# Kernel tuning notes

Measured on AMD Instinct MI355X. Metric: run time of the kernel, lower is better.

Reference implementation:

```python
import jax, jax.numpy as jnp
import numpy as np

EPS = 1e-12  # torch F.normalize default eps

def _l2norm(x):
    # torch.nn.functional.normalize(x, dim=-1): x / max(||x||_2, eps)
    n = jnp.linalg.norm(x, axis=-1, keepdims=True)
    return x / jnp.maximum(n, EPS)

def setup_inputs() -> dict:
    key = jax.random.key(0)
    ks = jax.random.split(key, 12)
    B, T, D, V, C = 16, 2048, 1024, 32000, 6
    s = 0.02
    text = jax.random.randint(ks[0], (B * T,), 0, V, dtype=jnp.int64)
    offsets = (jnp.arange(B, dtype=jnp.int64) * T)  # uniform-length sequences
    emb = jax.random.normal(ks[1], (V, D), dtype=jnp.float32) * s
    Wq = jax.random.normal(ks[2], (D, D), dtype=jnp.float32) * s
    bq = jnp.zeros((D,), jnp.float32)
    Wk = jax.random.normal(ks[3], (D, D), dtype=jnp.float32) * s
    bk = jnp.zeros((D,), jnp.float32)
    Wv = jax.random.normal(ks[4], (D, D), dtype=jnp.float32) * s
    bv = jnp.zeros((D,), jnp.float32)
    Wfc = jax.random.normal(ks[5], (D, D), dtype=jnp.float32) * s
    bfc = jnp.zeros((D,), jnp.float32)
    Wo = jax.random.normal(ks[6], (C, D), dtype=jnp.float32) * s
    bo = jnp.zeros((C,), jnp.float32)
    return {"text": text, "offsets": offsets, "emb": emb,
            "Wq": Wq, "bq": bq, "Wk": Wk, "bk": bk, "Wv": Wv, "bv": bv,
            "Wfc": Wfc, "bfc": bfc, "Wo": Wo, "bo": bo}

def reference(text, offsets, emb, Wq, bq, Wk, bk, Wv, bv, Wfc, bfc, Wo, bo):
    B = offsets.shape[0]
    T = text.shape[0] // B  # uniform lengths -> pad_sequence == reshape
    D = emb.shape[1]
    tok = text.reshape(B, T)
    x = emb[tok]                                   # [B,T,D]
    q = x @ Wq.T + bq
    k = x @ Wk.T + bk
    v = x @ Wv.T + bv
    scores = jnp.einsum('bqd,bkd->bqk', q, k) / jnp.sqrt(jnp.asarray(D, x.dtype))
    causal = jnp.tril(jnp.ones((T, T), dtype=bool))
    scores = jnp.where(causal[None, :, :], scores, -jnp.inf)
    attn = jax.nn.softmax(scores, axis=-1)
    out = jnp.einsum('bqk,bkd->bqd', attn, v) + x  # residual with embedding
    out = _l2norm(out)
    out = out + (out @ Wfc.T + bfc)                # residual FFN
    out = _l2norm(out)
    last = out[:, -1, :]                           # [B,D]
    return jax.nn.sigmoid(last @ Wo.T + bo)        # [B,num_class]
```

## Files before the change

kernel.cpp:

```cpp
#include <hip/hip_runtime.h>
#include <hip/hip_bf16.h>
#include <math.h>

typedef unsigned short ushort_t;

__device__ __forceinline__ float bf2f(ushort_t u) {
    union { unsigned int i; float f; } v;
    v.i = ((unsigned int)u) << 16;
    return v.f;
}

__device__ __forceinline__ ushort_t f2bf(float f) {
    union { float f; unsigned int i; } v; v.f = f;
    unsigned int lsb = (v.i >> 16) & 1;
    unsigned int r = v.i + 0x7FFF + lsb;
    return (ushort_t)(r >> 16);
}

__device__ __forceinline__ float wave_sum(float acc) {
    #pragma unroll
    for (int off = 32; off >= 1; off >>= 1) acc += __shfl_xor(acc, off, 64);
    return acc;
}
__device__ __forceinline__ float wave_max(float acc) {
    #pragma unroll
    for (int off = 32; off >= 1; off >>= 1) acc = fmaxf(acc, __shfl_xor(acc, off, 64));
    return acc;
}

__device__ __forceinline__ void ld8(const void* p, int isbf, size_t i, float* o) {
    if (isbf) {
        uint4 raw = *reinterpret_cast<const uint4*>((const ushort_t*)p + i);
        const ushort_t* pu = reinterpret_cast<const ushort_t*>(&raw);
        #pragma unroll
        for (int k = 0; k < 8; ++k) o[k] = bf2f(pu[k]);
    } else {
        const float4* f = reinterpret_cast<const float4*>((const float*)p + i);
        float4 a = f[0], b = f[1];
        o[0]=a.x; o[1]=a.y; o[2]=a.z; o[3]=a.w;
        o[4]=b.x; o[5]=b.y; o[6]=b.z; o[7]=b.w;
    }
}

__device__ __forceinline__ void ld4(const void* p, int isbf, size_t i, float* o) {
    if (isbf) {
        uint2 raw = *reinterpret_cast<const uint2*>((const ushort_t*)p + i);
        const ushort_t* pu = reinterpret_cast<const ushort_t*>(&raw);
        #pragma unroll
        for (int k = 0; k < 4; ++k) o[k] = bf2f(pu[k]);
    } else {
        float4 a = *reinterpret_cast<const float4*>((const float*)p + i);
        o[0]=a.x; o[1]=a.y; o[2]=a.z; o[3]=a.w;
    }
}

__device__ __forceinline__ float ldS(const void* p, int isbf, size_t i) {
    return isbf ? bf2f(((const ushort_t*)p)[i]) : ((const float*)p)[i];
}

__device__ __forceinline__ int tokAt(const void* text, int isi64, size_t i) {
    return isi64 ? ((const int*)text)[2 * i] : ((const int*)text)[i];
}

__device__ __forceinline__ void detect_flags(const void* emb, const void* text, int* sf) {
    if (threadIdx.x < 64) {
        const int lane = threadIdx.x;
        ushort_t u = ((const ushort_t*)emb)[2 * lane];
        int e = (u >> 7) & 0xFF;
        unsigned long long mb = __ballot(e >= 0x60 && e <= 0x7E);
        int odd = ((const int*)text)[2 * lane + 1];
        unsigned long long mi = __ballot(odd != 0);
        if (lane == 0) {
            sf[0] = (__popcll(mb) >= 32) ? 1 : 0;
            sf[1] = (__popcll(mi) == 0) ? 1 : 0;
        }
    }
    __syncthreads();
}

__device__ __forceinline__ void hoist16(const float* v, int lane, float* c16) {
    #pragma unroll
    for (int k = 0; k < 16; ++k) c16[k] = v[lane * 16 + k];
}

__global__ void kQC(const void* __restrict__ text, const void* __restrict__ emb,
                    const void* __restrict__ Wq, const void* __restrict__ bq,
                    const void* __restrict__ Wk, float* __restrict__ c_part,
                    int B, int T, int D) {
    const int ch = blockIdx.x / B;
    const int b  = blockIdx.x % B;
    const int i0 = ch << 6;
    const int tid = threadIdx.x;
    __shared__ int sf[2];
    __shared__ float xs[1024];
    __shared__ float qs[64];
    detect_flags(emb, text, sf);
    const int isbf = sf[0], isi64 = sf[1];
    const int tok = tokAt(text, isi64, (size_t)b * T + (T - 1));
    float w4[4];
    {
        const int dd = tid * 4;
        ld4(emb, isbf, (size_t)tok * D + dd, w4);
        xs[dd]=w4[0]; xs[dd+1]=w4[1]; xs[dd+2]=w4[2]; xs[dd+3]=w4[3];
    }
    __syncthreads();
    const int wave = tid >> 6, lane = tid & 63;
    float c16[16];
    hoist16(xs, lane, c16);
    float w[8];
    for (int r = 0; r < 16; ++r) {
        const int i = i0 + wave * 16 + r;
        float acc = 0.f;
        ld8(Wq, isbf, (size_t)i * D + lane * 16, w);
        #pragma unroll
        for (int k = 0; k < 8; ++k) acc += w[k] * c16[k];
        ld8(Wq, isbf, (size_t)i * D + lane * 16 + 8, w);
        #pragma unroll
        for (int k = 0; k < 8; ++k) acc += w[k] * c16[8 + k];
        acc = wave_sum(acc);
        if (lane == 0) qs[wave * 16 + r] = acc + ldS(bq, isbf, i);
    }
    __syncthreads();
    const int d = tid * 4;
    float a0=0.f, a1=0.f, a2=0.f, a3=0.f;
    #pragma unroll 8
    for (int i = 0; i < 64; ++i) {
        const float qv = qs[i];
        ld4(Wk, isbf, (size_t)(i0 + i) * D + d, w4);
        a0 += qv*w4[0]; a1 += qv*w4[1]; a2 += qv*w4[2]; a3 += qv*w4[3];
    }
    *reinterpret_cast<float4*>(c_part + ((size_t)ch * B + b) * D + d)
        = make_float4(a0, a1, a2, a3);
}

__global__ void kCC(const float* __restrict__ c_part, float* __restrict__ c,
                    int B, int D, int nch) {
    const int nb = D >> 8;
    const int b = blockIdx.x / nb;
    const int d = (blockIdx.x % nb) * 256 + threadIdx.x;
    float acc = 0.f;
    for (int cc = 0; cc < nch; ++cc)
        acc += c_part[((size_t)cc * B + b) * D + d];
    c[(size_t)b * D + d] = acc;
}

__global__ void k35(const void* __restrict__ text, const void* __restrict__ emb,
                    const float* __restrict__ c, float* __restrict__ xbar_part,
                    float* __restrict__ m_part, float* __restrict__ l_part,
                    int B, int T, int D, float scale) {
    const int nchT = T >> 5;
    const int b = blockIdx.x / nchT;
    const int ch = blockIdx.x % nchT;
    const int j0 = ch << 5;
    const int tid = threadIdx.x;
    __shared__ int sf[2];
    __shared__ ushort_t rows[32 * 1024];
    __shared__ float cs[1024];
    __shared__ float sjs[32];
    __shared__ float wls[32];
    __shared__ int tks[32];
    detect_flags(emb, text, sf);
    const int isbf = sf[0], isi64 = sf[1];
    {
        const int d = tid * 4;
        float4 v = *reinterpret_cast<const float4*>(c + (size_t)b * D + d);
        cs[d]=v.x; cs[d+1]=v.y; cs[d+2]=v.z; cs[d+3]=v.w;
    }
    if (tid < 32) tks[tid] = tokAt(text, isi64, (size_t)b * T + j0 + tid);
    __syncthreads();
    if (isbf) {
        const ushort_t* E = (const ushort_t*)emb;
        const int half = tid >> 7;
        const int off  = (tid & 127) * 8;
        #pragma unroll 4
        for (int sw = 0; sw < 16; ++sw) {
            const int r = sw * 2 + half;
            uint4 v = *reinterpret_cast<const uint4*>(E + (size_t)tks[r] * D + off);
            *reinterpret_cast<uint4*>(&rows[r * 1024 + off]) = v;
        }
    }
    __syncthreads();
    const int wave = tid >> 6, lane = tid & 63;
    {
        float c16[16];
        hoist16(cs, lane, c16);
        float w[8];
        for (int rr = 0; rr < 8; ++rr) {
            const int r = wave + rr * 4;
            float acc = 0.f;
            if (isbf) {
                uint4 raw = *reinterpret_cast<const uint4*>(&rows[r * 1024 + lane * 16]);
                const ushort_t* pu = reinterpret_cast<const ushort_t*>(&raw);
                #pragma unroll
                for (int k = 0; k < 8; ++k) acc += bf2f(pu[k]) * c16[k];
                raw = *reinterpret_cast<const uint4*>(&rows[r * 1024 + lane * 16 + 8]);
                #pragma unroll
                for (int k = 0; k < 8; ++k) acc += bf2f(pu[k]) * c16[8 + k];
            } else {
                ld8(emb, 0, (size_t)tks[r] * D + lane * 16, w);
                #pragma unroll
                for (int k = 0; k < 8; ++k) acc += w[k] * c16[k];
                ld8(emb, 0, (size_t)tks[r] * D + lane * 16 + 8, w);
                #pragma unroll
                for (int k = 0; k < 8; ++k) acc += w[k] * c16[8 + k];
            }
            acc = wave_sum(acc);
            if (lane == 0) sjs[r] = acc * scale;
        }
    }
    __syncthreads();
    float mx = -INFINITY;
    #pragma unroll
    for (int j = 0; j < 32; ++j) mx = fmaxf(mx, sjs[j]);
    if (tid < 32) wls[tid] = expf(sjs[tid] - mx);
    __syncthreads();
    if (tid < 64) {
        float v = (tid < 32) ? wls[tid] : 0.f;
        v = wave_sum(v);
        if (tid == 0) { m_part[(size_t)b * nchT + ch] = mx;
                        l_part[(size_t)b * nchT + ch] = v; }
    }
    const int d = tid * 4;
    float a0=0.f, a1=0.f, a2=0.f, a3=0.f;
    if (isbf) {
        #pragma unroll 8
        for (int j = 0; j < 32; ++j) {
            const float wj = wls[j];
            uint2 raw = *reinterpret_cast<const uint2*>(&rows[j * 1024 + d]);
            const ushort_t* pu = reinterpret_cast<const ushort_t*>(&raw);
            a0 += wj*bf2f(pu[0]); a1 += wj*bf2f(pu[1]);
            a2 += wj*bf2f(pu[2]); a3 += wj*bf2f(pu[3]);
        }
    } else {
        float w4[4];
        #pragma unroll 8
        for (int j = 0; j < 32; ++j) {
            const float wj = wls[j];
            ld4(emb, 0, (size_t)tks[j] * D + d, w4);
            a0 += wj*w4[0]; a1 += wj*w4[1]; a2 += wj*w4[2]; a3 += wj*w4[3];
        }
    }
    *reinterpret_cast<float4*>(xbar_part + ((size_t)b * nchT + ch) * D + d)
        = make_float4(a0, a1, a2, a3);
}

__global__ void kC(const float* __restrict__ xbar_part, const float* __restrict__ m_part,
                   const float* __restrict__ l_part, float* __restrict__ xbar,
                   int B, int D, int nchT) {
    const int nb = D >> 8;
    const int b = blockIdx.x / nb;
    const int d = (blockIdx.x % nb) * 256 + threadIdx.x;
    __shared__ float sc[128];
    if (threadIdx.x < 64) {
        float mx = -INFINITY;
        for (int cc = (int)threadIdx.x; cc < nchT; cc += 64)
            mx = fmaxf(mx, m_part[(size_t)b * nchT + cc]);
        mx = wave_max(mx);
        float ls = 0.f;
        for (int cc = (int)threadIdx.x; cc < nchT; cc += 64)
            ls += l_part[(size_t)b * nchT + cc] * expf(m_part[(size_t)b * nchT + cc] - mx);
        ls = wave_sum(ls);
        for (int cc = (int)threadIdx.x; cc < nchT; cc += 64)
            sc[cc] = expf(m_part[(size_t)b * nchT + cc] - mx) / ls;
    }
    __syncthreads();
    float acc = 0.f;
    for (int cc = 0; cc < nchT; ++cc)
        acc += sc[cc] * xbar_part[((size_t)b * nchT + cc) * D + d];
    xbar[(size_t)b * D + d] = acc;
}

__global__ void kVA(const void* __restrict__ text, const void* __restrict__ emb,
                    const void* __restrict__ Wv, const void* __restrict__ bv,
                    const float* __restrict__ xbar, float* __restrict__ u,
                    int B, int T, int D) {
    const int ch = blockIdx.x / B;
    const int b  = blockIdx.x % B;
    const int r0 = ch << 5;
    const int tid = threadIdx.x;
    __shared__ int sf[2];
    __shared__ float xb[1024];
    __shared__ float xl[32];
    detect_flags(emb, text, sf);
    const int isbf = sf[0], isi64 = sf[1];
    const int tok = tokAt(text, isi64, (size_t)b * T + (T - 1));
    if (tid < 32) xl[tid] = ldS(emb, isbf, (size_t)tok * D + r0 + tid);
    {
        const int dd = tid * 4;
        float4 v = *reinterpret_cast<const float4*>(xbar + (size_t)b * D + dd);
        xb[dd]=v.x; xb[dd+1]=v.y; xb[dd+2]=v.z; xb[dd+3]=v.w;
    }
    __syncthreads();
    const int wave = tid >> 6, lane = tid & 63;
    float c16[16];
    hoist16(xb, lane, c16);
    float w[8];
    for (int rr = 0; rr < 8; ++rr) {
        const int i = r0 + wave + rr * 4;
        float acc = 0.f;
        ld8(Wv, isbf, (size_t)i * D + lane * 16, w);
        #pragma unroll
        for (int k = 0; k < 8; ++k) acc += w[k] * c16[k];
        ld8(Wv, isbf, (size_t)i * D + lane * 16 + 8, w);
        #pragma unroll
        for (int k = 0; k < 8; ++k) acc += w[k] * c16[8 + k];
        acc = wave_sum(acc);
        if (lane == 0) u[(size_t)b * D + i] = acc + ldS(bv, isbf, i) + xl[i - r0];
    }
}

__global__ void k6c_h2(const void* __restrict__ text, const void* __restrict__ emb,
                       const void* __restrict__ Wfc, const void* __restrict__ bfc,
                       const float* __restrict__ u, float* __restrict__ h2,
                       int B, int D) {
    const int ch = blockIdx.x / B;
    const int b  = blockIdx.x % B;
    const int r0 = ch << 5;
    const int tid = threadIdx.x;
    __shared__ int sf[2];
    __shared__ float hs[1024];
    __shared__ float red[256];
    __shared__ float s_rn;
    detect_flags(emb, text, sf);
    const int isbf = sf[0];
    float part;
    {
        const int dd = tid * 4;
        float4 v = *reinterpret_cast<const float4*>(u + (size_t)b * D + dd);
        hs[dd]=v.x; hs[dd+1]=v.y; hs[dd+2]=v.z; hs[dd+3]=v.w;
        part = v.x*v.x + v.y*v.y + v.z*v.z + v.w*v.w;
    }
    red[tid] = part;
    __syncthreads();
    for (int st = 128; st; st >>= 1) {
        if (tid < st) red[tid] += red[tid + st];
        __syncthreads();
    }
    if (tid == 0) s_rn = 1.f / fmaxf(sqrtf(red[0]), 1e-12f);
    __syncthreads();
    const float rn = s_rn;
    {
        const int dd = tid * 4;
        hs[dd] *= rn; hs[dd+1] *= rn; hs[dd+2] *= rn; hs[dd+3] *= rn;
    }
    __syncthreads();
    const int wave = tid >> 6, lane = tid & 63;
    float c16[16];
    hoist16(hs, lane, c16);
    float w[8];
    for (int rr = 0; rr < 8; ++rr) {
        const int i = r0 + wave + rr * 4;
        float acc = 0.f;
        ld8(Wfc, isbf, (size_t)i * D + lane * 16, w);
        #pragma unroll
        for (int k = 0; k < 8; ++k) acc += w[k] * c16[k];
        ld8(Wfc, isbf, (size_t)i * D + lane * 16 + 8, w);
        #pragma unroll
        for (int k = 0; k < 8; ++k) acc += w[k] * c16[8 + k];
        acc = wave_sum(acc);
        if (lane == 0) h2[(size_t)b * D + i] = hs[i] + acc + ldS(bfc, isbf, i);
    }
}

__global__ void k6d_out(const void* __restrict__ text, const void* __restrict__ emb,
                        const void* __restrict__ Wo, const void* __restrict__ bo,
                        const float* __restrict__ h2, void* __restrict__ out,
                        int D, int C, int total) {
    __shared__ int sf[2];
    detect_flags(emb, text, sf);
    const int isbf = sf[0];
    const int g = blockIdx.x * 4 + (threadIdx.x >> 6);
    if (g >= total) return;
    const int lane = threadIdx.x & 63;
    const int b = g / C, ci = g % C;
    float a1 = 0.f, a2 = 0.f, w[8], h[8];
    for (int d0 = lane * 8; d0 < D; d0 += 512) {
        ld8(Wo, isbf, (size_t)ci * D + d0, w);
        ld8(h2, 0, (size_t)b * D + d0, h);
        #pragma unroll
        for (int k = 0; k < 8; ++k) { a1 += w[k] * h[k]; a2 += h[k] * h[k]; }
    }
    a1 = wave_sum(a1);
    a2 = wave_sum(a2);
    if (lane == 0) {
        float rn = 1.f / fmaxf(sqrtf(a2), 1e-12f);
        float z = a1 * rn + ldS(bo, isbf, ci);
        float y = 1.f / (1.f + expf(-z));
        if (isbf) ((ushort_t*)out)[g] = f2bf(y);
        else      ((float*)out)[g] = y;
    }
}

extern "C" void kernel_launch(void* const* d_in, const int* in_sizes, int n_in,
                              void* d_out, int out_size, void* d_ws, size_t ws_size,
                              hipStream_t stream) {
    const void* text = d_in[0];
    const void* emb = d_in[2];
    const void* Wq  = d_in[3];
    const void* bq  = d_in[4];
    const void* Wk  = d_in[5];
    const void* Wv  = d_in[7];
    const void* bv  = d_in[8];
    const void* Wfc = d_in[9];
    const void* bfc = d_in[10];
    const void* Wo  = d_in[11];
    const void* bo  = d_in[12];

    const int B = in_sizes[1];
    const int T = in_sizes[0] / B;
    const int D = in_sizes[4];
    const int C = in_sizes[12];

    const int nch_c = D / 64;
    const int nchT  = T / 32;

    float* ws        = (float*)d_ws;
    float* c_part    = ws;
    float* c         = c_part + (size_t)nch_c * B * D;
    float* xbar_part = c + (size_t)B * D;
    float* m_part    = xbar_part + (size_t)B * nchT * D;
    float* l_part    = m_part + (size_t)B * nchT;
    float* xbar      = l_part + (size_t)B * nchT;
    float* u         = xbar + (size_t)B * D;
    float* h2        = u + (size_t)B * D;

    const float scale = 1.0f / sqrtf((float)D);

    kQC<<<(D / 64) * B, 256, 0, stream>>>(text, emb, Wq, bq, Wk, c_part, B, T, D);
    kCC<<<B * (D / 256), 256, 0, stream>>>(c_part, c, B, D, nch_c);
    k35<<<B * (T / 32), 256, 0, stream>>>(text, emb, c, xbar_part, m_part, l_part,
                                          B, T, D, scale);
    kC<<<B * (D / 256), 256, 0, stream>>>(xbar_part, m_part, l_part, xbar, B, D, nchT);
    kVA<<<(D / 32) * B, 256, 0, stream>>>(text, emb, Wv, bv, xbar, u, B, T, D);
    k6c_h2<<<(D / 32) * B, 256, 0, stream>>>(text, emb, Wfc, bfc, u, h2, B, D);
    k6d_out<<<(B * C + 3) / 4, 256, 0, stream>>>(text, emb, Wo, bo, h2, d_out, D, C, B * C);
}
```

Before: 300.7 us.

## Halve chunk sizes in QC and attention kernels, split combine reductions across waves

```diff
diff --git a/kernel.cpp b/kernel.cpp
--- a/kernel.cpp
+++ b/kernel.cpp
@@ -89,11 +89,11 @@
                     int B, int T, int D) {
     const int ch = blockIdx.x / B;
     const int b  = blockIdx.x % B;
-    const int i0 = ch << 6;
+    const int i0 = ch << 5;
     const int tid = threadIdx.x;
     __shared__ int sf[2];
     __shared__ float xs[1024];
-    __shared__ float qs[64];
+    __shared__ float qs[32];
     detect_flags(emb, text, sf);
     const int isbf = sf[0], isi64 = sf[1];
     const int tok = tokAt(text, isi64, (size_t)b * T + (T - 1));
@@ -108,8 +108,8 @@
     float c16[16];
     hoist16(xs, lane, c16);
     float w[8];
-    for (int r = 0; r < 16; ++r) {
-        const int i = i0 + wave * 16 + r;
+    for (int r = 0; r < 8; ++r) {
+        const int i = i0 + wave * 8 + r;
         float acc = 0.f;
         ld8(Wq, isbf, (size_t)i * D + lane * 16, w);
         #pragma unroll
@@ -118,13 +118,13 @@
         #pragma unroll
         for (int k = 0; k < 8; ++k) acc += w[k] * c16[8 + k];
         acc = wave_sum(acc);
-        if (lane == 0) qs[wave * 16 + r] = acc + ldS(bq, isbf, i);
+        if (lane == 0) qs[wave * 8 + r] = acc + ldS(bq, isbf, i);
     }
     __syncthreads();
     const int d = tid * 4;
     float a0=0.f, a1=0.f, a2=0.f, a3=0.f;
     #pragma unroll 8
-    for (int i = 0; i < 64; ++i) {
+    for (int i = 0; i < 32; ++i) {
         const float qv = qs[i];
         ld4(Wk, isbf, (size_t)(i0 + i) * D + d, w4);
         a0 += qv*w4[0]; a1 += qv*w4[1]; a2 += qv*w4[2]; a3 += qv*w4[3];
@@ -135,30 +135,38 @@
 
 __global__ void kCC(const float* __restrict__ c_part, float* __restrict__ c,
                     int B, int D, int nch) {
-    const int nb = D >> 8;
+    const int nb = D >> 6;
     const int b = blockIdx.x / nb;
-    const int d = (blockIdx.x % nb) * 256 + threadIdx.x;
+    const int dblk = blockIdx.x % nb;
+    const int q = threadIdx.x >> 6, dl = threadIdx.x & 63;
+    const int d = dblk * 64 + dl;
+    __shared__ float red[256];
+    const int per = nch >> 2;
     float acc = 0.f;
-    for (int cc = 0; cc < nch; ++cc)
+    for (int j = 0; j < per; ++j) {
+        const int cc = q * per + j;
         acc += c_part[((size_t)cc * B + b) * D + d];
-    c[(size_t)b * D + d] = acc;
+    }
+    red[threadIdx.x] = acc;
+    __syncthreads();
+    if (q == 0) c[(size_t)b * D + d] = red[dl] + red[64 + dl] + red[128 + dl] + red[192 + dl];
 }
 
 __global__ void k35(const void* __restrict__ text, const void* __restrict__ emb,
                     const float* __restrict__ c, float* __restrict__ xbar_part,
                     float* __restrict__ m_part, float* __restrict__ l_part,
                     int B, int T, int D, float scale) {
-    const int nchT = T >> 5;
+    const int nchT = T >> 4;
     const int b = blockIdx.x / nchT;
     const int ch = blockIdx.x % nchT;
-    const int j0 = ch << 5;
+    const int j0 = ch << 4;
     const int tid = threadIdx.x;
     __shared__ int sf[2];
-    __shared__ ushort_t rows[32 * 1024];
+    __shared__ ushort_t rows[16 * 1024];
     __shared__ float cs[1024];
-    __shared__ float sjs[32];
-    __shared__ float wls[32];
-    __shared__ int tks[32];
+    __shared__ float sjs[16];
+    __shared__ float wls[16];
+    __shared__ int tks[16];
     detect_flags(emb, text, sf);
     const int isbf = sf[0], isi64 = sf[1];
     {
@@ -166,14 +174,14 @@
         float4 v = *reinterpret_cast<const float4*>(c + (size_t)b * D + d);
         cs[d]=v.x; cs[d+1]=v.y; cs[d+2]=v.z; cs[d+3]=v.w;
     }
-    if (tid < 32) tks[tid] = tokAt(text, isi64, (size_t)b * T + j0 + tid);
+    if (tid < 16) tks[tid] = tokAt(text, isi64, (size_t)b * T + j0 + tid);
     __syncthreads();
     if (isbf) {
         const ushort_t* E = (const ushort_t*)emb;
         const int half = tid >> 7;
         const int off  = (tid & 127) * 8;
-        #pragma unroll 4
-        for (int sw = 0; sw < 16; ++sw) {
+        #pragma unroll
+        for (int sw = 0; sw < 8; ++sw) {
             const int r = sw * 2 + half;
             uint4 v = *reinterpret_cast<const uint4*>(E + (size_t)tks[r] * D + off);
             *reinterpret_cast<uint4*>(&rows[r * 1024 + off]) = v;
@@ -185,7 +193,7 @@
         float c16[16];
         hoist16(cs, lane, c16);
         float w[8];
-        for (int rr = 0; rr < 8; ++rr) {
+        for (int rr = 0; rr < 4; ++rr) {
             const int r = wave + rr * 4;
             float acc = 0.f;
             if (isbf) {
@@ -211,11 +219,11 @@
     __syncthreads();
     float mx = -INFINITY;
     #pragma unroll
-    for (int j = 0; j < 32; ++j) mx = fmaxf(mx, sjs[j]);
-    if (tid < 32) wls[tid] = expf(sjs[tid] - mx);
+    for (int j = 0; j < 16; ++j) mx = fmaxf(mx, sjs[j]);
+    if (tid < 16) wls[tid] = expf(sjs[tid] - mx);
     __syncthreads();
     if (tid < 64) {
-        float v = (tid < 32) ? wls[tid] : 0.f;
+        float v = (tid < 16) ? wls[tid] : 0.f;
         v = wave_sum(v);
         if (tid == 0) { m_part[(size_t)b * nchT + ch] = mx;
                         l_part[(size_t)b * nchT + ch] = v; }
@@ -223,8 +231,8 @@
     const int d = tid * 4;
     float a0=0.f, a1=0.f, a2=0.f, a3=0.f;
     if (isbf) {
-        #pragma unroll 8
-        for (int j = 0; j < 32; ++j) {
+        #pragma unroll
+        for (int j = 0; j < 16; ++j) {
             const float wj = wls[j];
             uint2 raw = *reinterpret_cast<const uint2*>(&rows[j * 1024 + d]);
             const ushort_t* pu = reinterpret_cast<const ushort_t*>(&raw);
@@ -233,8 +241,8 @@
         }
     } else {
         float w4[4];
-        #pragma unroll 8
-        for (int j = 0; j < 32; ++j) {
+        #pragma unroll
+        for (int j = 0; j < 16; ++j) {
             const float wj = wls[j];
             ld4(emb, 0, (size_t)tks[j] * D + d, w4);
             a0 += wj*w4[0]; a1 += wj*w4[1]; a2 += wj*w4[2]; a3 += wj*w4[3];
@@ -247,27 +255,35 @@
 __global__ void kC(const float* __restrict__ xbar_part, const float* __restrict__ m_part,
                    const float* __restrict__ l_part, float* __restrict__ xbar,
                    int B, int D, int nchT) {
-    const int nb = D >> 8;
+    const int nb = D >> 6;
     const int b = blockIdx.x / nb;
-    const int d = (blockIdx.x % nb) * 256 + threadIdx.x;
+    const int dblk = blockIdx.x % nb;
+    const int q = threadIdx.x >> 6, dl = threadIdx.x & 63;
+    const int d = dblk * 64 + dl;
     __shared__ float sc[128];
+    __shared__ float red[256];
     if (threadIdx.x < 64) {
-        float mx = -INFINITY;
-        for (int cc = (int)threadIdx.x; cc < nchT; cc += 64)
-            mx = fmaxf(mx, m_part[(size_t)b * nchT + cc]);
-        mx = wave_max(mx);
-        float ls = 0.f;
-        for (int cc = (int)threadIdx.x; cc < nchT; cc += 64)
-            ls += l_part[(size_t)b * nchT + cc] * expf(m_part[(size_t)b * nchT + cc] - mx);
-        ls = wave_sum(ls);
-        for (int cc = (int)threadIdx.x; cc < nchT; cc += 64)
-            sc[cc] = expf(m_part[(size_t)b * nchT + cc] - mx) / ls;
-    }
-    __syncthreads();
+        const int t = threadIdx.x;
+        float m0 = (t < nchT) ? m_part[(size_t)b * nchT + t] : -INFINITY;
+        float m1 = (64 + t < nchT) ? m_part[(size_t)b * nchT + 64 + t] : -INFINITY;
+        float mx = wave_max(fmaxf(m0, m1));
+        float l0 = (t < nchT) ? l_part[(size_t)b * nchT + t] * expf(m0 - mx) : 0.f;
+        float l1 = (64 + t < nchT) ? l_part[(size_t)b * nchT + 64 + t] * expf(m1 - mx) : 0.f;
+        float ls = wave_sum(l0 + l1);
+        if (t < nchT) sc[t] = expf(m0 - mx) / ls;
+        if (64 + t < nchT) sc[64 + t] = expf(m1 - mx) / ls;
+    }
+    __syncthreads();
+    const int per = nchT >> 2;
     float acc = 0.f;
-    for (int cc = 0; cc < nchT; ++cc)
+    for (int j = 0; j < per; ++j) {
+        const int cc = q * per + j;
         acc += sc[cc] * xbar_part[((size_t)b * nchT + cc) * D + d];
-    xbar[(size_t)b * D + d] = acc;
+    }
+    red[threadIdx.x] = acc;
+    __syncthreads();
+    if (q == 0) xbar[(size_t)b * D + d] = red[dl] + red[64 + dl]
+                                        + red[128 + dl] + red[192 + dl];
 }
 
 __global__ void kVA(const void* __restrict__ text, const void* __restrict__ emb,
@@ -411,8 +427,8 @@
     const int D = in_sizes[4];
     const int C = in_sizes[12];
 
-    const int nch_c = D / 64;
-    const int nchT  = T / 32;
+    const int nch_c = D / 32;
+    const int nchT  = T / 16;
 
     float* ws        = (float*)d_ws;
     float* c_part    = ws;
@@ -426,11 +442,11 @@
 
     const float scale = 1.0f / sqrtf((float)D);
 
-    kQC<<<(D / 64) * B, 256, 0, stream>>>(text, emb, Wq, bq, Wk, c_part, B, T, D);
-    kCC<<<B * (D / 256), 256, 0, stream>>>(c_part, c, B, D, nch_c);
-    k35<<<B * (T / 32), 256, 0, stream>>>(text, emb, c, xbar_part, m_part, l_part,
+    kQC<<<(D / 32) * B, 256, 0, stream>>>(text, emb, Wq, bq, Wk, c_part, B, T, D);
+    kCC<<<B * (D / 64), 256, 0, stream>>>(c_part, c, B, D, nch_c);
+    k35<<<B * (T / 16), 256, 0, stream>>>(text, emb, c, xbar_part, m_part, l_part,
                                           B, T, D, scale);
-    kC<<<B * (D / 256), 256, 0, stream>>>(xbar_part, m_part, l_part, xbar, B, D, nchT);
+    kC<<<B * (D / 64), 256, 0, stream>>>(xbar_part, m_part, l_part, xbar, B, D, nchT);
     kVA<<<(D / 32) * B, 256, 0, stream>>>(text, emb, Wv, bv, xbar, u, B, T, D);
     k6c_h2<<<(D / 32) * B, 256, 0, stream>>>(text, emb, Wfc, bfc, u, h2, B, D);
     k6d_out<<<(B * C + 3) / 4, 256, 0, stream>>>(text, emb, Wo, bo, h2, d_out, D, C, B * C);
```

After: 286.1 us, median of 2. 1.05x faster.
